# Kernel tuning notes

Hardware: AMD Instinct MI355X
Metric: run time of the kernel (lower is better)

The kernel has to match this reference:

```python
import jax, jax.numpy as jnp
import numpy as np


def setup_inputs() -> dict:
    key = jax.random.key(0)
    ks = jax.random.split(key, 6)
    b, h, t, dh = 8, 8, 8192, 64
    buckets = 128
    return {
        "q": jax.random.normal(ks[0], (b, h, t, dh), jnp.float32),
        "k": jax.random.normal(ks[1], (b, h, t, dh), jnp.float32),
        "v": jax.random.normal(ks[2], (b, h, t, dh), jnp.float32),
        "sort_W": jax.random.normal(ks[3], (1, h, 2 * dh, buckets + 1), jnp.float32),
        "null_keys": jax.random.normal(ks[4], (h, 1, dh), jnp.float32),
        "null_values": jax.random.normal(ks[5], (h, 1, dh), jnp.float32),
    }


def _sinkhorn_causal_attention(q, k, v, sort_W, null_keys, null_values):
    b, h, t, dh = q.shape
    buckets = sort_W.shape[-1] - 1
    d = h * dh  # full model dim; torch code scales by d**-0.5 (not d_h)
    bsz = t // buckets
    hh = h // 2
    bh = b * h

    # rotate second half of heads left by bsz-1 along time
    def rot_heads(x, shift):
        return jnp.concatenate([x[:, :hh], jnp.roll(x[:, hh:], shift, axis=2)], axis=1)

    q = rot_heads(q, -(bsz - 1))
    k = rot_heads(k, -(bsz - 1))
    v = rot_heads(v, -(bsz - 1))

    qf = q.reshape(bh, t, dh)
    kf = k.reshape(bh, t, dh)
    vf = v.reshape(bh, t, dh)
    b_q = qf.reshape(bh, buckets, bsz, dh)
    b_k = kf.reshape(bh, buckets, bsz, dh)
    b_v = vf.reshape(bh, buckets, bsz, dh)

    # ---- CausalSimpleSortNet ----
    denom = jnp.arange(1, t + 1, dtype=kf.dtype)[None, :, None]
    k_cum = jnp.cumsum(kf, axis=1) / denom                      # cumavg over time
    k_r = jnp.concatenate([k_cum, kf], axis=-1)                  # [bh, t, 2dh]
    x = k_r.reshape(bh, buckets, bsz, 2 * dh)[:, :, 0]           # first token of each bucket
    R = jnp.einsum('bhud,hdc->bhuc', x.reshape(b, h, buckets, 2 * dh), sort_W[0])
    R = jax.nn.leaky_relu(R).reshape(bh, buckets, buckets + 1)

    # mask_reordering_matrix: forbid current/future buckets, softmax, strict lower-tri
    rows = jnp.arange(buckets)[:, None]
    cols = jnp.arange(buckets + 1)[None, :]
    neg = -jnp.finfo(R.dtype).max
    R = jnp.where(cols >= rows + 1, neg, R)
    R = jax.nn.softmax(R, axis=-1)
    R = jnp.where(cols < rows, R, jnp.zeros((), R.dtype))

    # zero_all_but_top (k=1) along last dim
    top_idx = jnp.argmax(R, axis=-1)                             # [bh, buckets]
    top_mask = cols[None] == top_idx[..., None]
    R = jnp.where(top_mask, R, jnp.zeros((), R.dtype))

    # null bucket prepended to keys/values
    b_null_k = jnp.broadcast_to(null_keys[None, :, None], (b, h, 1, bsz, dh)).reshape(bh, 1, bsz, dh)
    b_null_v = jnp.broadcast_to(null_values[None, :, None], (b, h, 1, bsz, dh)).reshape(bh, 1, bsz, dh)
    b_k_full = jnp.concatenate([b_null_k, b_k], axis=1)          # [bh, buckets+1, bsz, dh]
    b_v_full = jnp.concatenate([b_null_v, b_v], axis=1)

    # soft gather of routed buckets
    b_k_r = jnp.einsum('buv,bvtd->butd', R, b_k_full)
    b_v_r = jnp.einsum('buv,bvtd->butd', R, b_v_full)
    b_k2 = jnp.concatenate([b_k_r, b_k], axis=2)                 # [bh, buckets, 2bsz, dh]
    b_v2 = jnp.concatenate([b_v_r, b_v], axis=2)

    dots = jnp.einsum('buie,buje->buij', b_q, b_k2) * (d ** -0.5)

    # attention mask
    i = jnp.arange(bsz)[:, None]
    j = jnp.arange(bsz)[None, :]
    base = jnp.concatenate([jnp.ones((bsz, bsz), bool), j <= i], axis=-1)  # [bsz, 2bsz]
    head_rot = (jnp.arange(h) >= hh)[None, :, None, None, None]
    last_bkt = (jnp.arange(buckets) == buckets - 1)[None, None, :, None, None]
    row_idx = jnp.arange(bsz)[None, None, None, :, None]
    col_idx = jnp.arange(2 * bsz)[None, None, None, None, :]
    special = (col_idx <= bsz) & (row_idx >= 1)
    mask = base[None, None, None] & ~(head_rot & last_bkt & special)
    mask = jnp.broadcast_to(mask, (b, h, buckets, bsz, 2 * bsz)).reshape(bh, buckets, bsz, 2 * bsz)

    dots = jnp.where(mask, dots, -jnp.finfo(dots.dtype).max)
    attn = jax.nn.softmax(dots, axis=-1)
    out = jnp.einsum('buij,buje->buie', attn, b_v2)              # [bh, buckets, bsz, dh]
    out = out.reshape(b, h, t, dh)
    out = jnp.concatenate([out[:, :hh], jnp.roll(out[:, hh:], bsz - 1, axis=2)], axis=1)
    return out


def reference(q, k, v, sort_W, null_keys, null_values):
    return _sinkhorn_causal_attention(q, k, v, sort_W, null_keys, null_values)
```

## Files before the change

### kernel.cpp

```cpp
#include <hip/hip_runtime.h>

#define T     8192
#define DH    64
#define TMASK 8191
#define SCALE 0.044194173824159216f
#define NEGF  -3.402823466e38f

typedef __attribute__((ext_vector_type(8))) short bf16x8;
typedef __attribute__((ext_vector_type(4))) float f32x4;

static __device__ __forceinline__ unsigned short f2bf(float f) {
  unsigned int u = __float_as_uint(f);
  u += 0x7fffu + ((u >> 16) & 1u);
  return (unsigned short)(u >> 16);
}

__global__ void __launch_bounds__(256) seg_sums_kernel(
    const float* __restrict__ k, float* __restrict__ segs) {
  int bid = blockIdx.x;
  int bhi = bid >> 5;
  int ch  = bid & 31;
  int hd  = bhi & 7;
  bool rot = hd >= 4;
  int tid = threadIdx.x;
  int sgl = tid >> 6;
  int c   = tid & 63;
  int sg  = ch * 4 + sgl;
  const float* kb = k + (size_t)bhi * T * DH;
  float sum = 0.f;
  int t0 = sg * 64;
  for (int s = 0; s < 64; ++s) {
    int t  = t0 + s;
    int st = rot ? ((t + 63) & TMASK) : t;
    sum += kb[(size_t)st * DH + c];
  }
  segs[((size_t)bhi * 128 + sg) * 64 + c] = sum;
}

__global__ void __launch_bounds__(256) route_kernel(
    const float* __restrict__ k, const float* __restrict__ sortW,
    const float* __restrict__ segs,
    int* __restrict__ routeIdx, float* __restrict__ routeP) {
  __shared__ float sSeg[128 * 64];
  __shared__ float sX[16 * 128];
  int bid = blockIdx.x;
  int bhi = bid >> 3;
  int u0  = (bid & 7) * 16;
  int hd  = bhi & 7;
  bool rot = hd >= 4;
  int tid = threadIdx.x;
  const float* kb = k + (size_t)bhi * T * DH;
  const float* sg = segs + (size_t)bhi * 128 * 64;

#pragma unroll
  for (int it = 0; it < 8; ++it) {
    int f4 = (it * 256 + tid) * 4;
    *(float4*)(sSeg + f4) = *(const float4*)(sg + f4);
  }
  {
    int r = tid >> 4, c4 = (tid & 15) << 2;
    int t = (u0 + r) * 64;
    int st = rot ? ((t + 63) & TMASK) : t;
    *(float4*)(sX + r * 128 + 64 + c4) = *(const float4*)(kb + (size_t)st * DH + c4);
  }
  __syncthreads();
  {
    int r = tid >> 4, c4 = (tid & 15) << 2;
    int u = u0 + r;
    float4 run = make_float4(0.f, 0.f, 0.f, 0.f);
    for (int uu = 0; uu < u; ++uu) {
      float4 sv = *(const float4*)(sSeg + uu * 64 + c4);
      run.x += sv.x; run.y += sv.y; run.z += sv.z; run.w += sv.w;
    }
    float4 first = *(const float4*)(sX + r * 128 + 64 + c4);
    float den = (float)(u * 64 + 1);
    float4 cum = make_float4((run.x + first.x) / den, (run.y + first.y) / den,
                             (run.z + first.z) / den, (run.w + first.w) / den);
    *(float4*)(sX + r * 128 + c4) = cum;
  }
  __syncthreads();

  int ty = tid >> 4, tx = tid & 15;
  int u = u0 + ty;
  const float* Wh = sortW + (size_t)hd * 128 * 129;
  float z[8] = {0.f, 0.f, 0.f, 0.f, 0.f, 0.f, 0.f, 0.f};
  for (int d = 0; d < 128; ++d) {
    float xv = sX[ty * 128 + d];
    const float* wr = Wh + (size_t)d * 129 + tx;
#pragma unroll
    for (int j = 0; j < 8; ++j) z[j] = fmaf(xv, wr[j * 16], z[j]);
  }
  float l[8];
  float mx = NEGF;
#pragma unroll
  for (int j = 0; j < 8; ++j) {
    int c = tx + 16 * j;
    float lv = z[j] >= 0.f ? z[j] : 0.01f * z[j];
    l[j] = lv;
    if (c <= u) mx = fmaxf(mx, lv);
  }
  for (int off = 1; off < 16; off <<= 1) mx = fmaxf(mx, __shfl_xor(mx, off));
  float se = 0.f;
#pragma unroll
  for (int j = 0; j < 8; ++j) {
    int c = tx + 16 * j;
    if (c <= u) se += __expf(l[j] - mx);
  }
  for (int off = 1; off < 16; off <<= 1) se += __shfl_xor(se, off);
  float bv = NEGF; int bi = 0x7fffffff;
#pragma unroll
  for (int j = 0; j < 8; ++j) {
    int c = tx + 16 * j;
    if (c < u && (l[j] > bv || (l[j] == bv && c < bi))) { bv = l[j]; bi = c; }
  }
  for (int off = 1; off < 16; off <<= 1) {
    float ov = __shfl_xor(bv, off); int oi = __shfl_xor(bi, off);
    if (ov > bv || (ov == bv && oi < bi)) { bv = ov; bi = oi; }
  }
  if (tx == 0) {
    if (u == 0) { routeIdx[bhi * 128] = 0; routeP[bhi * 128] = 0.f; }
    else {
      routeIdx[bhi * 128 + u] = bi;
      routeP[bhi * 128 + u]   = __expf(bv - mx) / se;
    }
  }
}

__global__ void __launch_bounds__(256, 3) attn_kernel(
    const float* __restrict__ q, const float* __restrict__ k,
    const float* __restrict__ v,
    const float* __restrict__ nullk, const float* __restrict__ nullv,
    const int* __restrict__ routeIdx, const float* __restrict__ routeP,
    float* __restrict__ out) {
  __shared__ __align__(16) unsigned short smem[22528];
  unsigned short* sQ  = smem;
  unsigned short* sK  = smem + 4608;
  unsigned short* sVt = smem + 13824;
  unsigned short* sP  = smem;

  const int bid = blockIdx.x;
  const int u   = bid & 127;
  const int bhi = bid >> 7;
  const int hd  = bhi & 7;
  const bool rot = hd >= 4;
  const int tid = threadIdx.x;
  const float* qb = q + (size_t)bhi * T * DH;
  const float* kb = k + (size_t)bhi * T * DH;
  const float* vb = v + (size_t)bhi * T * DH;
  float* ob = out + (size_t)bhi * T * DH;
  const int   ridx = routeIdx[bhi * 128 + u];
  const float p    = routeP[bhi * 128 + u];
  const float* nkh = nullk + hd * DH;
  const float* nvh = nullv + hd * DH;

#pragma unroll
  for (int it = 0; it < 4; ++it) {
    int flat = it * 256 + tid;
    int row = flat >> 4, c4 = (flat & 15) << 2;
    int t  = u * 64 + row;
    int st = rot ? ((t + 63) & TMASK) : t;
    float4 qv = *(const float4*)(qb + (size_t)st * DH + c4);
    ushort4 o4;
    o4.x = f2bf(qv.x * SCALE); o4.y = f2bf(qv.y * SCALE);
    o4.z = f2bf(qv.z * SCALE); o4.w = f2bf(qv.w * SCALE);
    *(ushort4*)(sQ + row * 72 + c4) = o4;
  }
#pragma unroll
  for (int it = 0; it < 8; ++it) {
    int flat = it * 256 + tid;
    int row = flat >> 4, c4 = (flat & 15) << 2;
    float4 kv;
    if (row < 64) {
      if (ridx == 0) kv = *(const float4*)(nkh + c4);
      else {
        int t = (ridx - 1) * 64 + row;
        int st = rot ? ((t + 63) & TMASK) : t;
        kv = *(const float4*)(kb + (size_t)st * DH + c4);
      }
      kv.x *= p; kv.y *= p; kv.z *= p; kv.w *= p;
    } else {
      int t = u * 64 + (row - 64);
      int st = rot ? ((t + 63) & TMASK) : t;
      kv = *(const float4*)(kb + (size_t)st * DH + c4);
    }
    ushort4 o4;
    o4.x = f2bf(kv.x); o4.y = f2bf(kv.y); o4.z = f2bf(kv.z); o4.w = f2bf(kv.w);
    *(ushort4*)(sK + row * 72 + c4) = o4;
  }
#pragma unroll
  for (int it = 0; it < 8; ++it) {
    int flat = it * 256 + tid;
    int row = flat >> 4, c4 = (flat & 15) << 2;
    float4 vv;
    if (row < 64) {
      if (ridx == 0) vv = *(const float4*)(nvh + c4);
      else {
        int t = (ridx - 1) * 64 + row;
        int st = rot ? ((t + 63) & TMASK) : t;
        vv = *(const float4*)(vb + (size_t)st * DH + c4);
      }
      vv.x *= p; vv.y *= p; vv.z *= p; vv.w *= p;
    } else {
      int t = u * 64 + (row - 64);
      int st = rot ? ((t + 63) & TMASK) : t;
      vv = *(const float4*)(vb + (size_t)st * DH + c4);
    }
    sVt[(c4 + 0) * 136 + row] = f2bf(vv.x);
    sVt[(c4 + 1) * 136 + row] = f2bf(vv.y);
    sVt[(c4 + 2) * 136 + row] = f2bf(vv.z);
    sVt[(c4 + 3) * 136 + row] = f2bf(vv.w);
  }
  __syncthreads();

  const int lane = tid & 63;
  const int w    = tid >> 6;
  const int col  = lane & 15;
  const int quad = lane >> 4;
  const int kofs = quad * 8;
  const int mrow = w * 16 + col;

  f32x4 acc[8];
#pragma unroll
  for (int j = 0; j < 8; ++j) acc[j] = (f32x4){0.f, 0.f, 0.f, 0.f};
  bf16x8 aq0 = *(const bf16x8*)(sQ + mrow * 72 + 0  + kofs);
  bf16x8 aq1 = *(const bf16x8*)(sQ + mrow * 72 + 32 + kofs);
#pragma unroll
  for (int j = 0; j < 8; ++j) {
    bf16x8 b0 = *(const bf16x8*)(sK + (j * 16 + col) * 72 + 0  + kofs);
    acc[j] = __builtin_amdgcn_mfma_f32_16x16x32_bf16(aq0, b0, acc[j], 0, 0, 0);
    bf16x8 b1 = *(const bf16x8*)(sK + (j * 16 + col) * 72 + 32 + kofs);
    acc[j] = __builtin_amdgcn_mfma_f32_16x16x32_bf16(aq1, b1, acc[j], 0, 0, 0);
  }

  const bool spec = rot && (u == 127);
#pragma unroll
  for (int reg = 0; reg < 4; ++reg) {
    int r = w * 16 + quad * 4 + reg;
    float mx = -1e30f;
#pragma unroll
    for (int j = 0; j < 8; ++j) {
      int c = j * 16 + col;
      bool vis = (c < 64) || ((c - 64) <= r);
      if (spec && r >= 1 && c <= 64) vis = false;
      float val = vis ? acc[j][reg] : -1e30f;
      acc[j][reg] = val;
      mx = fmaxf(mx, val);
    }
#pragma unroll
    for (int off = 1; off < 16; off <<= 1) mx = fmaxf(mx, __shfl_xor(mx, off));
    float s = 0.f;
#pragma unroll
    for (int j = 0; j < 8; ++j) {
      float e = __expf(acc[j][reg] - mx);
      acc[j][reg] = e; s += e;
    }
#pragma unroll
    for (int off = 1; off < 16; off <<= 1) s += __shfl_xor(s, off);
    float inv = 1.f / s;
#pragma unroll
    for (int j = 0; j < 8; ++j) acc[j][reg] *= inv;
  }

  __syncthreads();
#pragma unroll
  for (int j = 0; j < 8; ++j)
#pragma unroll
    for (int reg = 0; reg < 4; ++reg)
      sP[(w * 16 + quad * 4 + reg) * 136 + j * 16 + col] = f2bf(acc[j][reg]);
  __syncthreads();

  f32x4 oacc[4];
#pragma unroll
  for (int jt = 0; jt < 4; ++jt) oacc[jt] = (f32x4){0.f, 0.f, 0.f, 0.f};
#pragma unroll
  for (int ks = 0; ks < 4; ++ks) {
    bf16x8 ap = *(const bf16x8*)(sP + mrow * 136 + ks * 32 + kofs);
#pragma unroll
    for (int jt = 0; jt < 4; ++jt) {
      bf16x8 bv = *(const bf16x8*)(sVt + (jt * 16 + col) * 136 + ks * 32 + kofs);
      oacc[jt] = __builtin_amdgcn_mfma_f32_16x16x32_bf16(ap, bv, oacc[jt], 0, 0, 0);
    }
  }

#pragma unroll
  for (int reg = 0; reg < 4; ++reg) {
    int r = w * 16 + quad * 4 + reg;
    int t = u * 64 + r;
    int st = rot ? ((t + 63) & TMASK) : t;
    float* orow = ob + (size_t)st * DH;
#pragma unroll
    for (int jt = 0; jt < 4; ++jt)
      orow[jt * 16 + col] = oacc[jt][reg];
  }
}

extern "C" void kernel_launch(void* const* d_in, const int* in_sizes, int n_in,
                              void* d_out, int out_size, void* d_ws, size_t ws_size,
                              hipStream_t stream) {
  const float* q     = (const float*)d_in[0];
  const float* k     = (const float*)d_in[1];
  const float* v     = (const float*)d_in[2];
  const float* sortW = (const float*)d_in[3];
  const float* nullk = (const float*)d_in[4];
  const float* nullv = (const float*)d_in[5];
  float* out = (float*)d_out;

  float* segs     = (float*)d_ws;
  int*   routeIdx = (int*)((char*)d_ws + (size_t)64 * 128 * 64 * 4);
  float* routeP   = (float*)((char*)d_ws + (size_t)64 * 128 * 64 * 4 + 32768);

  seg_sums_kernel<<<2048, 256, 0, stream>>>(k, segs);
  route_kernel<<<512, 256, 0, stream>>>(k, sortW, segs, routeIdx, routeP);
  attn_kernel<<<8192, 256, 0, stream>>>(q, k, v, nullk, nullv,
                                        routeIdx, routeP, out);
}
```

Measured before the change: 474.5 us.

## Vectorize seg sums, load Q into registers, swizzle V transpose, remap blocks

seg_sums now uses float4 loads with four segments per wave and a quarter of the blocks. The attention kernel loads Q straight from global into MFMA register fragments and drops the sQ shared buffer. It also writes V transposed through packed ushort4 stores into an XOR-swizzled layout, packs P stores with a lane shuffle, remaps block IDs, and raises the occupancy hint to 4 blocks. The aim is less LDS use, fewer bank conflicts and fewer narrow stores, at the cost of more index arithmetic and possible register pressure.

```diff
diff --git a/kernel.cpp b/kernel.cpp
--- a/kernel.cpp
+++ b/kernel.cpp
@@ -18,23 +18,27 @@
 __global__ void __launch_bounds__(256) seg_sums_kernel(
     const float* __restrict__ k, float* __restrict__ segs) {
   int bid = blockIdx.x;
-  int bhi = bid >> 5;
-  int ch  = bid & 31;
+  int bhi = bid >> 3;
+  int ch  = bid & 7;
   int hd  = bhi & 7;
   bool rot = hd >= 4;
   int tid = threadIdx.x;
-  int sgl = tid >> 6;
-  int c   = tid & 63;
-  int sg  = ch * 4 + sgl;
+  int lane = tid & 63;
+  int wv   = tid >> 6;
+  int sg   = ch * 16 + wv * 4 + (lane >> 4);
+  int c4   = (lane & 15) << 2;
   const float* kb = k + (size_t)bhi * T * DH;
-  float sum = 0.f;
   int t0 = sg * 64;
+  float s0 = 0.f, s1 = 0.f, s2 = 0.f, s3 = 0.f;
+#pragma unroll 8
   for (int s = 0; s < 64; ++s) {
     int t  = t0 + s;
     int st = rot ? ((t + 63) & TMASK) : t;
-    sum += kb[(size_t)st * DH + c];
-  }
-  segs[((size_t)bhi * 128 + sg) * 64 + c] = sum;
+    float4 x = *(const float4*)(kb + (size_t)st * DH + c4);
+    s0 += x.x; s1 += x.y; s2 += x.z; s3 += x.w;
+  }
+  *(float4*)(segs + ((size_t)bhi * 128 + sg) * 64 + c4) =
+      make_float4(s0, s1, s2, s3);
 }
 
 __global__ void __launch_bounds__(256) route_kernel(
@@ -84,6 +88,7 @@
   int u = u0 + ty;
   const float* Wh = sortW + (size_t)hd * 128 * 129;
   float z[8] = {0.f, 0.f, 0.f, 0.f, 0.f, 0.f, 0.f, 0.f};
+#pragma unroll 4
   for (int d = 0; d < 128; ++d) {
     float xv = sX[ty * 128 + d];
     const float* wr = Wh + (size_t)d * 129 + tx;
@@ -126,19 +131,19 @@
   }
 }
 
-__global__ void __launch_bounds__(256, 3) attn_kernel(
+__global__ void __launch_bounds__(256, 4) attn_kernel(
     const float* __restrict__ q, const float* __restrict__ k,
     const float* __restrict__ v,
     const float* __restrict__ nullk, const float* __restrict__ nullv,
     const int* __restrict__ routeIdx, const float* __restrict__ routeP,
     float* __restrict__ out) {
-  __shared__ __align__(16) unsigned short smem[22528];
-  unsigned short* sQ  = smem;
-  unsigned short* sK  = smem + 4608;
-  unsigned short* sVt = smem + 13824;
+  __shared__ __align__(16) unsigned short smem[17408];
+  unsigned short* sK  = smem;
+  unsigned short* sVt = smem + 9216;
   unsigned short* sP  = smem;
 
-  const int bid = blockIdx.x;
+  const int bid0 = blockIdx.x;
+  const int bid  = ((bid0 & 7) << 10) | (bid0 >> 3);
   const int u   = bid & 127;
   const int bhi = bid >> 7;
   const int hd  = bhi & 7;
@@ -153,18 +158,32 @@
   const float* nkh = nullk + hd * DH;
   const float* nvh = nullv + hd * DH;
 
-#pragma unroll
-  for (int it = 0; it < 4; ++it) {
-    int flat = it * 256 + tid;
-    int row = flat >> 4, c4 = (flat & 15) << 2;
-    int t  = u * 64 + row;
+  const int lane = tid & 63;
+  const int w    = tid >> 6;
+  const int col  = lane & 15;
+  const int quad = lane >> 4;
+  const int kofs = quad * 8;
+  const int mrow = w * 16 + col;
+
+  bf16x8 aq0, aq1;
+  {
+    int t  = u * 64 + mrow;
     int st = rot ? ((t + 63) & TMASK) : t;
-    float4 qv = *(const float4*)(qb + (size_t)st * DH + c4);
-    ushort4 o4;
-    o4.x = f2bf(qv.x * SCALE); o4.y = f2bf(qv.y * SCALE);
-    o4.z = f2bf(qv.z * SCALE); o4.w = f2bf(qv.w * SCALE);
-    *(ushort4*)(sQ + row * 72 + c4) = o4;
-  }
+    const float* qr = qb + (size_t)st * DH + kofs;
+    float4 a0 = *(const float4*)(qr + 0);
+    float4 a1 = *(const float4*)(qr + 4);
+    float4 a2 = *(const float4*)(qr + 32);
+    float4 a3 = *(const float4*)(qr + 36);
+    aq0[0] = (short)f2bf(a0.x * SCALE); aq0[1] = (short)f2bf(a0.y * SCALE);
+    aq0[2] = (short)f2bf(a0.z * SCALE); aq0[3] = (short)f2bf(a0.w * SCALE);
+    aq0[4] = (short)f2bf(a1.x * SCALE); aq0[5] = (short)f2bf(a1.y * SCALE);
+    aq0[6] = (short)f2bf(a1.z * SCALE); aq0[7] = (short)f2bf(a1.w * SCALE);
+    aq1[0] = (short)f2bf(a2.x * SCALE); aq1[1] = (short)f2bf(a2.y * SCALE);
+    aq1[2] = (short)f2bf(a2.z * SCALE); aq1[3] = (short)f2bf(a2.w * SCALE);
+    aq1[4] = (short)f2bf(a3.x * SCALE); aq1[5] = (short)f2bf(a3.y * SCALE);
+    aq1[6] = (short)f2bf(a3.z * SCALE); aq1[7] = (short)f2bf(a3.w * SCALE);
+  }
+
 #pragma unroll
   for (int it = 0; it < 8; ++it) {
     int flat = it * 256 + tid;
@@ -187,43 +206,56 @@
     o4.x = f2bf(kv.x); o4.y = f2bf(kv.y); o4.z = f2bf(kv.z); o4.w = f2bf(kv.w);
     *(ushort4*)(sK + row * 72 + c4) = o4;
   }
-#pragma unroll
-  for (int it = 0; it < 8; ++it) {
+
+#pragma unroll
+  for (int it = 0; it < 2; ++it) {
     int flat = it * 256 + tid;
-    int row = flat >> 4, c4 = (flat & 15) << 2;
-    float4 vv;
-    if (row < 64) {
-      if (ridx == 0) vv = *(const float4*)(nvh + c4);
-      else {
-        int t = (ridx - 1) * 64 + row;
+    int tok4 = flat >> 4;
+    int d4   = (flat & 15) << 2;
+    int tb   = tok4 * 4;
+    float va[4][4];
+    if (tb < 64) {
+      if (ridx == 0) {
+        float4 nv = *(const float4*)(nvh + d4);
+        float n0 = nv.x * p, n1 = nv.y * p, n2 = nv.z * p, n3 = nv.w * p;
+#pragma unroll
+        for (int jj = 0; jj < 4; ++jj) {
+          va[jj][0] = n0; va[jj][1] = n1; va[jj][2] = n2; va[jj][3] = n3;
+        }
+      } else {
+#pragma unroll
+        for (int jj = 0; jj < 4; ++jj) {
+          int t = (ridx - 1) * 64 + tb + jj;
+          int st = rot ? ((t + 63) & TMASK) : t;
+          float4 x = *(const float4*)(vb + (size_t)st * DH + d4);
+          va[jj][0] = x.x * p; va[jj][1] = x.y * p;
+          va[jj][2] = x.z * p; va[jj][3] = x.w * p;
+        }
+      }
+    } else {
+#pragma unroll
+      for (int jj = 0; jj < 4; ++jj) {
+        int t = u * 64 + (tb - 64) + jj;
         int st = rot ? ((t + 63) & TMASK) : t;
-        vv = *(const float4*)(vb + (size_t)st * DH + c4);
+        float4 x = *(const float4*)(vb + (size_t)st * DH + d4);
+        va[jj][0] = x.x; va[jj][1] = x.y; va[jj][2] = x.z; va[jj][3] = x.w;
       }
-      vv.x *= p; vv.y *= p; vv.z *= p; vv.w *= p;
-    } else {
-      int t = u * 64 + (row - 64);
-      int st = rot ? ((t + 63) & TMASK) : t;
-      vv = *(const float4*)(vb + (size_t)st * DH + c4);
-    }
-    sVt[(c4 + 0) * 136 + row] = f2bf(vv.x);
-    sVt[(c4 + 1) * 136 + row] = f2bf(vv.y);
-    sVt[(c4 + 2) * 136 + row] = f2bf(vv.z);
-    sVt[(c4 + 3) * 136 + row] = f2bf(vv.w);
-  }
-  __syncthreads();
-
-  const int lane = tid & 63;
-  const int w    = tid >> 6;
-  const int col  = lane & 15;
-  const int quad = lane >> 4;
-  const int kofs = quad * 8;
-  const int mrow = w * 16 + col;
+    }
+    int chunk = tok4 >> 1, ph = tok4 & 1;
+#pragma unroll
+    for (int dd = 0; dd < 4; ++dd) {
+      int n = d4 + dd;
+      ushort4 o;
+      o.x = f2bf(va[0][dd]); o.y = f2bf(va[1][dd]);
+      o.z = f2bf(va[2][dd]); o.w = f2bf(va[3][dd]);
+      *(ushort4*)(sVt + n * 128 + ((chunk ^ (n & 15)) << 3) + (ph << 2)) = o;
+    }
+  }
+  __syncthreads();
 
   f32x4 acc[8];
 #pragma unroll
   for (int j = 0; j < 8; ++j) acc[j] = (f32x4){0.f, 0.f, 0.f, 0.f};
-  bf16x8 aq0 = *(const bf16x8*)(sQ + mrow * 72 + 0  + kofs);
-  bf16x8 aq1 = *(const bf16x8*)(sQ + mrow * 72 + 32 + kofs);
 #pragma unroll
   for (int j = 0; j < 8; ++j) {
     bf16x8 b0 = *(const bf16x8*)(sK + (j * 16 + col) * 72 + 0  + kofs);
@@ -263,10 +295,17 @@
 
   __syncthreads();
 #pragma unroll
-  for (int j = 0; j < 8; ++j)
-#pragma unroll
-    for (int reg = 0; reg < 4; ++reg)
-      sP[(w * 16 + quad * 4 + reg) * 136 + j * 16 + col] = f2bf(acc[j][reg]);
+  for (int j = 0; j < 8; ++j) {
+#pragma unroll
+    for (int reg = 0; reg < 4; ++reg) {
+      unsigned int mybf = f2bf(acc[j][reg]);
+      unsigned int obf  = (unsigned int)__shfl_xor((int)mybf, 1);
+      if ((col & 1) == 0) {
+        int r = w * 16 + quad * 4 + reg;
+        *(unsigned int*)(sP + r * 136 + j * 16 + col) = mybf | (obf << 16);
+      }
+    }
+  }
   __syncthreads();
 
   f32x4 oacc[4];
@@ -277,7 +316,8 @@
     bf16x8 ap = *(const bf16x8*)(sP + mrow * 136 + ks * 32 + kofs);
 #pragma unroll
     for (int jt = 0; jt < 4; ++jt) {
-      bf16x8 bv = *(const bf16x8*)(sVt + (jt * 16 + col) * 136 + ks * 32 + kofs);
+      int n = jt * 16 + col;
+      bf16x8 bv = *(const bf16x8*)(sVt + n * 128 + (((ks * 4 + quad) ^ col) << 3));
       oacc[jt] = __builtin_amdgcn_mfma_f32_16x16x32_bf16(ap, bv, oacc[jt], 0, 0, 0);
     }
   }
@@ -309,7 +349,7 @@
   int*   routeIdx = (int*)((char*)d_ws + (size_t)64 * 128 * 64 * 4);
   float* routeP   = (float*)((char*)d_ws + (size_t)64 * 128 * 64 * 4 + 32768);
 
-  seg_sums_kernel<<<2048, 256, 0, stream>>>(k, segs);
+  seg_sums_kernel<<<512, 256, 0, stream>>>(k, segs);
   route_kernel<<<512, 256, 0, stream>>>(k, sortW, segs, routeIdx, routeP);
   attn_kernel<<<8192, 256, 0, stream>>>(q, k, v, nullk, nullv,
                                         routeIdx, routeP, out);
```

Result: faster. 454.6 us (-4.2%).
